# Kernel optimization log

Measured on AMD Instinct MI355X. Metric: run time of the kernel, lower is better.

Reference implementation:

```python
import jax, jax.numpy as jnp
import numpy as np

B, DETER, STOCH, ACT_DIM, HIDDEN, BLOCKS, DEMB = 4096, 4096, 1024, 32, 512, 8, 16
EPS = 1e-4
OUT_B = DETER // BLOCKS            # 512 per-block output
IN_B0 = 4 * HIDDEN + OUT_B          # 2560 per-block input of first hidden block-GEMM


def rmsnorm(x, g):
    return x * jax.lax.rsqrt(jnp.mean(x * x, axis=-1, keepdims=True) + EPS) * g


def setup_inputs() -> dict:
    key = jax.random.key(0)
    ks = jax.random.split(key, 16)
    n = lambda k, s: (jax.random.normal(k, s, jnp.float32) * 0.02)
    return {
        'stoch': jax.random.normal(ks[0], (B, STOCH), jnp.float32),
        'deter': jax.random.normal(ks[1], (B, DETER), jnp.float32),
        'action': jax.random.normal(ks[2], (B, ACT_DIM), jnp.float32),
        'd_emb': jax.random.normal(ks[3], (B, DEMB), jnp.float32),
        # four input branches: Linear -> RMSNorm -> SiLU
        'W0': n(ks[4], (DETER, HIDDEN)), 'b0': jnp.zeros(HIDDEN), 'g0': jnp.ones(HIDDEN),
        'W1': n(ks[5], (STOCH, HIDDEN)), 'b1': jnp.zeros(HIDDEN), 'g1': jnp.ones(HIDDEN),
        'W2': n(ks[6], (ACT_DIM, HIDDEN)), 'b2': jnp.zeros(HIDDEN), 'g2': jnp.ones(HIDDEN),
        'W3': n(ks[7], (DEMB, HIDDEN)), 'b3': jnp.zeros(HIDDEN), 'g3': jnp.ones(HIDDEN),
        # block-diagonal hidden layers (dynlayers=2)
        'Wh0': n(ks[8], (BLOCKS, IN_B0, OUT_B)), 'bh0': jnp.zeros(DETER), 'gh0': jnp.ones(DETER),
        'Wh1': n(ks[9], (BLOCKS, OUT_B, OUT_B)), 'bh1': jnp.zeros(DETER), 'gh1': jnp.ones(DETER),
        # block-diagonal GRU gate projection: deter -> 3*deter
        'Wg': n(ks[10], (BLOCKS, OUT_B, 3 * OUT_B)), 'bg': jnp.zeros(3 * DETER),
    }


def reference(stoch, deter, action, d_emb,
              W0, b0, g0, W1, b1, g1, W2, b2, g2, W3, b3, g3,
              Wh0, bh0, gh0, Wh1, bh1, gh1, Wg, bg):
    act = jax.nn.silu
    Bsz = action.shape[0]
    stoch = stoch.reshape(Bsz, -1)
    # action / clip(|action|, min=1).detach()
    action = action / jax.lax.stop_gradient(jnp.maximum(jnp.abs(action), 1.0))

    x0 = act(rmsnorm(deter @ W0 + b0, g0))
    x1 = act(rmsnorm(stoch @ W1 + b1, g1))
    x2 = act(rmsnorm(action @ W2 + b2, g2))
    x3 = act(rmsnorm(d_emb @ W3 + b3, g3))
    x = jnp.concatenate([x0, x1, x2, x3], axis=-1)          # [B, 4H]

    xg = jnp.broadcast_to(x[:, None, :], (Bsz, BLOCKS, 4 * HIDDEN))
    dg = deter.reshape(Bsz, BLOCKS, OUT_B)                   # flat2group(deter)
    h = jnp.concatenate([dg, xg], axis=-1)                   # [B, blocks, in_b0]

    # hidden layer 0: BlockLinear -> RMSNorm(full width) -> act
    h = jnp.einsum('bgi,gio->bgo', h, Wh0).reshape(Bsz, DETER) + bh0
    h = act(rmsnorm(h, gh0))
    # hidden layer 1
    h = jnp.einsum('bgi,gio->bgo', h.reshape(Bsz, BLOCKS, OUT_B), Wh1).reshape(Bsz, DETER) + bh1
    h = act(rmsnorm(h, gh1))

    # GRU gates via block-diagonal GEMM: [B, blocks, 3*out_b]
    gates = jnp.einsum('bgi,gio->bgo', h.reshape(Bsz, BLOCKS, OUT_B), Wg).reshape(Bsz, 3 * DETER) + bg
    gg = gates.reshape(Bsz, BLOCKS, 3 * OUT_B)
    reset = gg[..., :OUT_B].reshape(Bsz, DETER)
    cand = gg[..., OUT_B:2 * OUT_B].reshape(Bsz, DETER)
    update = gg[..., 2 * OUT_B:].reshape(Bsz, DETER)

    reset = jax.nn.sigmoid(reset)
    cand = jnp.tanh(reset * cand)
    update = jax.nn.sigmoid(update - 1.0)
    return update * cand + (1.0 - update) * deter
```

## Files before the change

### kernel.cpp

```cpp
#include <hip/hip_runtime.h>
#include <hip/hip_bf16.h>
#include <cstdint>

typedef __bf16 bf16x8 __attribute__((ext_vector_type(8)));
typedef float f32x4 __attribute__((ext_vector_type(4)));
typedef unsigned short u16x8 __attribute__((ext_vector_type(8)));
typedef unsigned short u16x4 __attribute__((ext_vector_type(4)));

__device__ __forceinline__ unsigned short f2bf(float f) {
  unsigned int u = __float_as_uint(f);
  u += 0x7FFFu + ((u >> 16) & 1u);
  return (unsigned short)(u >> 16);
}
__device__ __forceinline__ float bf2f(unsigned short h) {
  return __uint_as_float(((unsigned int)h) << 16);
}
__device__ __forceinline__ float frcp_(float x) { return __builtin_amdgcn_rcpf(x); }
__device__ __forceinline__ float sigmoid_fast(float x) { return frcp_(1.f + __expf(-x)); }
__device__ __forceinline__ float tanh_fast(float x) { return 1.f - 2.f * frcp_(__expf(2.f * x) + 1.f); }
__device__ __forceinline__ float siluf_(float x) { return x * sigmoid_fast(x); }

#define GLOAD_LDS16(gsrc, ldst) \
  __builtin_amdgcn_global_load_lds((const __attribute__((address_space(1))) void*)(gsrc), \
                                   (__attribute__((address_space(3))) void*)(ldst), 16, 0, 0)

#define S_BARRIER() asm volatile("s_barrier" ::: "memory")
#define WAIT_LGKM0() do { asm volatile("s_waitcnt lgkmcnt(0)" ::: "memory"); \
                          __builtin_amdgcn_sched_barrier(0); } while (0)

__device__ __forceinline__ void xcd_tile(int& x, int& y, int& z) {
  const int gx = gridDim.x, gy = gridDim.y;
  const int nwg = gx * gy * gridDim.z;
  const int lin = (blockIdx.z * gy + blockIdx.y) * gx + blockIdx.x;
  const int cpx = nwg >> 3;
  const int t = (lin & 7) * cpx + (lin >> 3);
  x = t % gx;
  const int r = t / gx;
  y = r % gy;
  z = r / gy;
}

template<int F32>
__device__ __forceinline__ void gemm8_core(
    const unsigned short* __restrict__ A1, int lda1, int K1,
    const unsigned short* __restrict__ A2, int lda2, int K2,
    const unsigned short* __restrict__ Bt, int ldb,
    void* __restrict__ C, int ldc,
    int tm, int tn, unsigned short* lds)
{
  const int tid = threadIdx.x;
  const int lane = tid & 63;
  const int wave = tid >> 6;
  const int wm = (wave >> 2) * 128;
  const int wn = (wave & 3) * 64;
  const int frow = lane & 15;
  const int chunk16 = (lane >> 4) * 16;
  const int nt = (K1 + K2) >> 5;

  auto stageA = [&](unsigned short* dstA, int ktBase) {
    const unsigned short* Ab; int alda, kloc;
    if (ktBase >= K1) { Ab = A2; alda = lda2; kloc = ktBase - K1; }
    else              { Ab = A1; alda = lda1; kloc = ktBase; }
#pragma unroll
    for (int j = 0; j < 2; ++j) {
      int o = j * 8192 + tid * 16;
      int so = o ^ (((o >> 7) & 3) << 4);
      int row = so >> 6, cb = so & 63;
      GLOAD_LDS16(Ab + (long long)(tm + row) * alda + kloc + (cb >> 1),
                  (char*)dstA + j * 8192 + wave * 1024);
    }
  };
  auto stageB = [&](unsigned short* dstB, int ktBase) {
#pragma unroll
    for (int j = 0; j < 2; ++j) {
      int o = j * 8192 + tid * 16;
      int so = o ^ (((o >> 7) & 3) << 4);
      int row = so >> 6, cb = so & 63;
      GLOAD_LDS16(Bt + (long long)(tn + row) * ldb + ktBase + (cb >> 1),
                  (char*)dstB + j * 8192 + wave * 1024);
    }
  };
  auto ldswz = [&](const unsigned short* rg, int row) -> bf16x8 {
    int o = row * 64 + chunk16;
    o ^= ((o >> 7) & 3) << 4;
    return *(const bf16x8*)((const char*)rg + o);
  };

  f32x4 acc[8][4] = {};

  unsigned short* pc = lds;
  unsigned short* pn = lds + 16384;
  unsigned short* pf = lds + 32768;

  stageA(pc, 0); stageB(pc + 8192, 0);
  stageA(pn, 32); stageB(pn + 8192, 32);
  asm volatile("s_waitcnt vmcnt(4)" ::: "memory");
  S_BARRIER();

  for (int T = 0; T < nt; ++T) {
    const unsigned short* A_ = pc;
    const unsigned short* B_ = pc + 8192;
    bf16x8 av[4], bv[4];
#pragma unroll
    for (int j = 0; j < 4; ++j) bv[j] = ldswz(B_, wn + j * 16 + frow);
#pragma unroll
    for (int i = 0; i < 4; ++i) av[i] = ldswz(A_, wm + i * 16 + frow);
    if (T + 2 < nt) stageA(pf, (T + 2) * 32);
    S_BARRIER();
    WAIT_LGKM0();
    __builtin_amdgcn_s_setprio(1);
#pragma unroll
    for (int i = 0; i < 4; ++i)
#pragma unroll
      for (int j = 0; j < 4; ++j)
        acc[i][j] = __builtin_amdgcn_mfma_f32_16x16x32_bf16(av[i], bv[j], acc[i][j], 0, 0, 0);
    __builtin_amdgcn_s_setprio(0);
    __builtin_amdgcn_sched_barrier(0);
    S_BARRIER();
#pragma unroll
    for (int i = 0; i < 4; ++i) av[i] = ldswz(A_, wm + 64 + i * 16 + frow);
    if (T + 2 < nt) {
      stageB(pf + 8192, (T + 2) * 32);
      asm volatile("s_waitcnt vmcnt(4)" ::: "memory");
    } else if (T + 1 < nt) {
      asm volatile("s_waitcnt vmcnt(0)" ::: "memory");
    }
    S_BARRIER();
    WAIT_LGKM0();
    __builtin_amdgcn_s_setprio(1);
#pragma unroll
    for (int i = 0; i < 4; ++i)
#pragma unroll
      for (int j = 0; j < 4; ++j)
        acc[4 + i][j] = __builtin_amdgcn_mfma_f32_16x16x32_bf16(av[i], bv[j], acc[4 + i][j], 0, 0, 0);
    __builtin_amdgcn_s_setprio(0);
    __builtin_amdgcn_sched_barrier(0);
    S_BARRIER();
    unsigned short* t = pc; pc = pn; pn = pf; pf = t;
  }

  const int cr = (lane >> 4) * 4;
  const int cc = lane & 15;
#pragma unroll
  for (int mf = 0; mf < 8; ++mf) {
    const int r0 = tm + wm + mf * 16 + cr;
#pragma unroll
    for (int j = 0; j < 4; ++j) {
      const int col = tn + wn + j * 16 + cc;
#pragma unroll
      for (int i = 0; i < 4; ++i) {
        if (F32) ((float*)C)[(long long)(r0 + i) * ldc + col] = acc[mf][j][i];
        else ((unsigned short*)C)[(long long)(r0 + i) * ldc + col] = f2bf(acc[mf][j][i]);
      }
    }
  }
}

__global__ __launch_bounds__(512, 2) void gemm8(
    const unsigned short* __restrict__ A1, int lda1, long long a1_bs, int K1,
    const unsigned short* __restrict__ A2, int lda2, int K2,
    const unsigned short* __restrict__ Bt, int ldb, long long bt_bs,
    unsigned short* __restrict__ C, int ldc, long long c_bs)
{
  __shared__ unsigned short lds[3 * 16384];
  int tx, ty, g;
  xcd_tile(tx, ty, g);
  gemm8_core<0>(A1 + (long long)g * a1_bs, lda1, K1, A2, lda2, K2,
                Bt + (long long)g * bt_bs, ldb,
                C + (long long)g * c_bs, ldc,
                ty * 256, tx * 256, lds);
}

struct BCfg { const unsigned short* A; int lda; const unsigned short* Bt; int ldb; float* C; };
struct BPack { BCfg c[5]; };
__global__ __launch_bounds__(512, 2) void gemm8_branch(BPack p) {
  __shared__ unsigned short lds[3 * 16384];
  int tx, ty, z;
  xcd_tile(tx, ty, z);
  BCfg c = p.c[z];
  gemm8_core<1>(c.A, c.lda, 1024, nullptr, 0, 0, c.Bt, c.ldb, c.C, 512,
                ty * 256, tx * 256, lds);
}

__global__ __launch_bounds__(512, 2) void gemm_gru(
    const unsigned short* __restrict__ hB,
    const unsigned short* __restrict__ Wgt,
    const float* __restrict__ bg,
    const unsigned short* __restrict__ deterB,
    float* __restrict__ out)
{
  __shared__ unsigned short lds[3 * 14336];
  int txi, tyi, g;
  xcd_tile(txi, tyi, g);
  const int tm = tyi * 256;
  const int tn = txi * 192;
  const unsigned short* A  = hB + g * 512;
  const unsigned short* Bt = Wgt + (long long)g * 1536 * 512;
  const int tid = threadIdx.x, lane = tid & 63, wave = tid >> 6;
  const int wm = (wave >> 2) * 128;
  const int wv = wave & 3;
  const int frow = lane & 15, chunk16 = (lane >> 4) * 16;
  const bool wlow = (wave < 4);
  const int nt = 16;

  auto stageA = [&](unsigned short* buf, int kt) {
#pragma unroll
    for (int j = 0; j < 2; ++j) {
      int o = j * 8192 + tid * 16;
      int so = o ^ (((o >> 7) & 3) << 4);
      int row = so >> 6, cb = so & 63;
      GLOAD_LDS16(A + (long long)(tm + row) * 4096 + kt + (cb >> 1),
                  (char*)buf + j * 8192 + wave * 1024);
    }
  };
  auto stageB = [&](unsigned short* buf, int kt) {
    char* bb = (char*)(buf + 8192);
    {
      int o = tid * 16;
      int so = o ^ (((o >> 7) & 3) << 4);
      int row = so >> 6, cb = so & 63;
      GLOAD_LDS16(Bt + (long long)(tn + row) * 512 + kt + (cb >> 1),
                  bb + wave * 1024);
    }
    if (tid < 256) {
      int o = 8192 + tid * 16;
      int so = o ^ (((o >> 7) & 3) << 4);
      int row = so >> 6, cb = so & 63;
      GLOAD_LDS16(Bt + (long long)(tn + row) * 512 + kt + (cb >> 1),
                  bb + 8192 + wave * 1024);
    }
  };
  auto ldA = [&](const unsigned short* buf, int row) -> bf16x8 {
    int o = row * 64 + chunk16; o ^= ((o >> 7) & 3) << 4;
    return *(const bf16x8*)((const char*)buf + o);
  };
  auto ldB = [&](const unsigned short* buf, int nf) -> bf16x8 {
    int row = wv * 48 + nf * 16 + frow;
    int o = row * 64 + chunk16; o ^= ((o >> 7) & 3) << 4;
    return *(const bf16x8*)((const char*)(buf + 8192) + o);
  };
  auto wait_pref = [&]() {
    if (wlow) asm volatile("s_waitcnt vmcnt(4)" ::: "memory");
    else      asm volatile("s_waitcnt vmcnt(3)" ::: "memory");
  };

  f32x4 acc[8][3] = {};

  unsigned short* pc = lds;
  unsigned short* pn = lds + 14336;
  unsigned short* pf = lds + 28672;

  stageA(pc, 0); stageB(pc, 0);
  stageA(pn, 32); stageB(pn, 32);
  wait_pref();
  S_BARRIER();

  for (int T = 0; T < nt; ++T) {
    bf16x8 av[4], bv[3];
#pragma unroll
    for (int j = 0; j < 3; ++j) bv[j] = ldB(pc, j);
#pragma unroll
    for (int i = 0; i < 4; ++i) av[i] = ldA(pc, wm + i * 16 + frow);
    if (T + 2 < nt) stageA(pf, (T + 2) * 32);
    S_BARRIER();
    WAIT_LGKM0();
    __builtin_amdgcn_s_setprio(1);
#pragma unroll
    for (int i = 0; i < 4; ++i)
#pragma unroll
      for (int j = 0; j < 3; ++j)
        acc[i][j] = __builtin_amdgcn_mfma_f32_16x16x32_bf16(av[i], bv[j], acc[i][j], 0, 0, 0);
    __builtin_amdgcn_s_setprio(0);
    __builtin_amdgcn_sched_barrier(0);
    S_BARRIER();
#pragma unroll
    for (int i = 0; i < 4; ++i) av[i] = ldA(pc, wm + 64 + i * 16 + frow);
    if (T + 2 < nt) {
      stageB(pf, (T + 2) * 32);
      wait_pref();
    } else if (T + 1 < nt) {
      asm volatile("s_waitcnt vmcnt(0)" ::: "memory");
    }
    S_BARRIER();
    WAIT_LGKM0();
    __builtin_amdgcn_s_setprio(1);
#pragma unroll
    for (int i = 0; i < 4; ++i)
#pragma unroll
      for (int j = 0; j < 3; ++j)
        acc[4 + i][j] = __builtin_amdgcn_mfma_f32_16x16x32_bf16(av[i], bv[j], acc[4 + i][j], 0, 0, 0);
    __builtin_amdgcn_s_setprio(0);
    __builtin_amdgcn_sched_barrier(0);
    S_BARRIER();
    unsigned short* t = pc; pc = pn; pn = pf; pf = t;
  }

  const int cr = (lane >> 4) * 4, cc = lane & 15;
  const int o_col = (txi * 4 + wv) * 16 + cc;
  const int gcol = g * 512 + o_col;
  const float bgr = bg[g * 1536 + o_col];
  const float bgc = bg[g * 1536 + 512 + o_col];
  const float bgu = bg[g * 1536 + 1024 + o_col];
#pragma unroll
  for (int mf = 0; mf < 8; ++mf) {
    const int r0 = tm + wm + mf * 16 + cr;
#pragma unroll
    for (int i = 0; i < 4; ++i) {
      const long long off = (long long)(r0 + i) * 4096 + gcol;
      float dt = bf2f(deterB[off]);
      float reset = sigmoid_fast(acc[mf][0][i] + bgr);
      float cand  = tanh_fast(reset * (acc[mf][1][i] + bgc));
      float upd   = sigmoid_fast(acc[mf][2][i] + bgu - 1.f);
      out[off] = upd * cand + (1.f - upd) * dt;
    }
  }
}

__global__ void cvt2_bf16_k(const float* __restrict__ sa, unsigned short* __restrict__ da, int n4a,
                            const float* __restrict__ sb, unsigned short* __restrict__ db, int n4b) {
  int i = blockIdx.x * 256 + threadIdx.x;
  const float* s; unsigned short* d;
  if (i < n4a) { s = sa; d = da; }
  else { i -= n4a; if (i >= n4b) return; s = sb; d = db; }
  float4 v = ((const float4*)s)[i];
  u16x4 o;
  o.x = f2bf(v.x); o.y = f2bf(v.y); o.z = f2bf(v.z); o.w = f2bf(v.w);
  ((u16x4*)d)[i] = o;
}

__global__ void transpose_cvt(const float* __restrict__ src, unsigned short* __restrict__ dst,
                              int R, int C) {
  __shared__ float t[32][33];
  const long long bOff = (long long)blockIdx.z * R * C;
  src += bOff; dst += bOff;
  const int c0 = blockIdx.x * 32, r0 = blockIdx.y * 32;
  const int tx = threadIdx.x, ty = threadIdx.y;
#pragma unroll
  for (int i = 0; i < 4; ++i) {
    int r = r0 + ty + i * 8, c = c0 + tx;
    if (r < R && c < C) t[ty + i * 8][tx] = src[(long long)r * C + c];
  }
  __syncthreads();
#pragma unroll
  for (int i = 0; i < 4; ++i) {
    int c = c0 + ty + i * 8, r = r0 + tx;
    if (r < R && c < C) dst[(long long)c * R + r] = f2bf(t[tx][ty + i * 8]);
  }
}

__global__ void transpose_wg(const float* __restrict__ src, unsigned short* __restrict__ dst) {
  __shared__ float t[32][33];
  const int gz = blockIdx.z;
  src += (long long)gz * 512 * 1536;
  dst += (long long)gz * 1536 * 512;
  const int c0 = blockIdx.x * 32, r0 = blockIdx.y * 32;
  const int tx = threadIdx.x, ty = threadIdx.y;
#pragma unroll
  for (int i = 0; i < 4; ++i)
    t[ty + i * 8][tx] = src[(long long)(r0 + ty + i * 8) * 1536 + c0 + tx];
  __syncthreads();
#pragma unroll
  for (int i = 0; i < 4; ++i) {
    int c = c0 + ty + i * 8;
    int gate = c >> 9, o = c & 511;
    int nn = (o >> 4) * 48 + gate * 16 + (o & 15);
    dst[(long long)nn * 512 + r0 + tx] = f2bf(t[tx][ty + i * 8]);
  }
}

__global__ __launch_bounds__(256) void branch_epi_k(
    const float* __restrict__ yP0, const float* __restrict__ yP1,
    const float* __restrict__ b0, const float* __restrict__ g0,
    const float* __restrict__ b1, const float* __restrict__ g1,
    const float* __restrict__ action, const float* __restrict__ demb,
    const float* __restrict__ W2, const float* __restrict__ b2, const float* __restrict__ g2,
    const float* __restrict__ W3, const float* __restrict__ b3, const float* __restrict__ g3,
    unsigned short* __restrict__ x)
{
  const int row = blockIdx.x, br = blockIdx.y;
  const int tid = threadIdx.x, lane = tid & 63, wave = tid >> 6;
  __shared__ float red[4];
  __shared__ float a[32];
  float v0, v1;
  const float* gg;
  if (br == 0) {
    const float* p = yP0 + (long long)row * 512;
    v0 = b0[tid]; v1 = b0[tid + 256];
#pragma unroll
    for (int c = 0; c < 4; ++c) {
      v0 += p[c * 2097152 + tid];
      v1 += p[c * 2097152 + tid + 256];
    }
    gg = g0;
  } else if (br == 1) {
    const float* p = yP1 + (long long)row * 512;
    v0 = b1[tid] + p[tid];
    v1 = b1[tid + 256] + p[tid + 256];
    gg = g1;
  } else {
    const int K = (br == 3) ? 16 : 32;
    const float* W  = (br == 3) ? W3 : W2;
    const float* bb = (br == 3) ? b3 : b2;
    gg = (br == 3) ? g3 : g2;
    if (tid < K) {
      float t = (br == 3) ? demb[(long long)row * 16 + tid]
                          : action[(long long)row * 32 + tid];
      if (br == 2) t = t / fmaxf(fabsf(t), 1.f);
      a[tid] = t;
    }
    __syncthreads();
    v0 = bb[tid]; v1 = bb[tid + 256];
    for (int k = 0; k < K; ++k) {
      float av = a[k];
      v0 += av * W[k * 512 + tid];
      v1 += av * W[k * 512 + tid + 256];
    }
  }
  float ss = v0 * v0 + v1 * v1;
  for (int o = 32; o > 0; o >>= 1) ss += __shfl_xor(ss, o);
  if (lane == 0) red[wave] = ss;
  __syncthreads();
  float ms = (red[0] + red[1] + red[2] + red[3]) * (1.f / 512.f);
  float sc = rsqrtf(ms + 1e-4f);
  unsigned short* xr = x + (long long)row * 2048 + br * 512;
  xr[tid]       = f2bf(siluf_(v0 * sc * gg[tid]));
  xr[tid + 256] = f2bf(siluf_(v1 * sc * gg[tid + 256]));
}

__global__ __launch_bounds__(256) void epi_full_k(
    const unsigned short* __restrict__ y, const float* __restrict__ bias,
    const float* __restrict__ gw, unsigned short* __restrict__ h)
{
  const int row = blockIdx.x;
  __shared__ float red[4];
  const int tid = threadIdx.x, lane = tid & 63, wave = tid >> 6;
  const u16x8* yv = (const u16x8*)(y + (long long)row * 4096);
  u16x8 ta = yv[tid], tb = yv[256 + tid];
  float ba[8], bb8[8];
  *(float4*)&ba[0]  = *(const float4*)&bias[tid * 8];
  *(float4*)&ba[4]  = *(const float4*)&bias[tid * 8 + 4];
  *(float4*)&bb8[0] = *(const float4*)&bias[(256 + tid) * 8];
  *(float4*)&bb8[4] = *(const float4*)&bias[(256 + tid) * 8 + 4];
  float fa[8], fb[8];
  float ss = 0.f;
#pragma unroll
  for (int e = 0; e < 8; ++e) {
    fa[e] = bf2f(ta[e]) + ba[e];  ss += fa[e] * fa[e];
    fb[e] = bf2f(tb[e]) + bb8[e]; ss += fb[e] * fb[e];
  }
  for (int o = 32; o > 0; o >>= 1) ss += __shfl_xor(ss, o);
  if (lane == 0) red[wave] = ss;
  __syncthreads();
  float ms = (red[0] + red[1] + red[2] + red[3]) * (1.f / 4096.f);
  float sc = rsqrtf(ms + 1e-4f);
  float ga[8], gb8[8];
  *(float4*)&ga[0]  = *(const float4*)&gw[tid * 8];
  *(float4*)&ga[4]  = *(const float4*)&gw[tid * 8 + 4];
  *(float4*)&gb8[0] = *(const float4*)&gw[(256 + tid) * 8];
  *(float4*)&gb8[4] = *(const float4*)&gw[(256 + tid) * 8 + 4];
  u16x8 oa, ob;
#pragma unroll
  for (int e = 0; e < 8; ++e) {
    oa[e] = f2bf(siluf_(fa[e] * sc * ga[e]));
    ob[e] = f2bf(siluf_(fb[e] * sc * gb8[e]));
  }
  u16x8* hv = (u16x8*)(h + (long long)row * 4096);
  hv[tid] = oa;
  hv[256 + tid] = ob;
}

extern "C" void kernel_launch(void* const* d_in, const int* in_sizes, int n_in,
                              void* d_out, int out_size, void* d_ws, size_t ws_size,
                              hipStream_t stream) {
  const float* stoch  = (const float*)d_in[0];
  const float* deter  = (const float*)d_in[1];
  const float* action = (const float*)d_in[2];
  const float* demb   = (const float*)d_in[3];
  const float* W0 = (const float*)d_in[4];
  const float* b0 = (const float*)d_in[5];
  const float* g0 = (const float*)d_in[6];
  const float* W1 = (const float*)d_in[7];
  const float* b1 = (const float*)d_in[8];
  const float* g1 = (const float*)d_in[9];
  const float* W2 = (const float*)d_in[10];
  const float* b2 = (const float*)d_in[11];
  const float* g2 = (const float*)d_in[12];
  const float* W3 = (const float*)d_in[13];
  const float* b3 = (const float*)d_in[14];
  const float* g3 = (const float*)d_in[15];
  const float* Wh0 = (const float*)d_in[16];
  const float* bh0 = (const float*)d_in[17];
  const float* gh0 = (const float*)d_in[18];
  const float* Wh1 = (const float*)d_in[19];
  const float* bh1 = (const float*)d_in[20];
  const float* gh1 = (const float*)d_in[21];
  const float* Wg  = (const float*)d_in[22];
  const float* bg  = (const float*)d_in[23];
  float* out = (float*)d_out;

  char* ws = (char*)d_ws;
  unsigned short* deterB = (unsigned short*)(ws + 0);
  unsigned short* stochB = (unsigned short*)(ws + 33554432);
  unsigned short* W0t    = (unsigned short*)(ws + 41943040);
  unsigned short* W1t    = (unsigned short*)(ws + 46137344);
  unsigned short* xB     = (unsigned short*)(ws + 47185920);
  float*          yP0    = (float*)(ws + 63963136);
  unsigned short* yB     = (unsigned short*)(ws + 63963136);
  float*          yP1    = (float*)(ws + 97517568);
  unsigned short* Wh0t   = (unsigned short*)(ws + 105906176);
  unsigned short* Wgt    = (unsigned short*)(ws + 105906176);
  unsigned short* Wh1t   = (unsigned short*)(ws + 126877696);
  unsigned short* hB     = (unsigned short*)(ws + 134217728);
  (void)in_sizes; (void)n_in; (void)out_size; (void)ws_size;

  dim3 b256(256);
  dim3 b512(512);
  dim3 tb(32, 8);
  cvt2_bf16_k<<<dim3(20480), b256, 0, stream>>>(deter, deterB, 4194304,
                                                stoch, stochB, 1048576);
  transpose_cvt<<<dim3(16, 128, 1), tb, 0, stream>>>(W0,  W0t,  4096, 512);
  transpose_cvt<<<dim3(16, 32, 1),  tb, 0, stream>>>(W1,  W1t,  1024, 512);
  {
    BPack p;
    for (int z = 0; z < 4; ++z)
      p.c[z] = { deterB + z * 1024, 4096, W0t + z * 1024, 4096, yP0 + (long long)z * 2097152 };
    p.c[4] = { stochB, 1024, W1t, 1024, yP1 };
    gemm8_branch<<<dim3(2, 16, 5), b512, 0, stream>>>(p);
  }
  branch_epi_k<<<dim3(4096, 4), b256, 0, stream>>>(yP0, yP1, b0, g0, b1, g1,
                                                   action, demb, W2, b2, g2, W3, b3, g3, xB);
  transpose_cvt<<<dim3(16, 80, 8),  tb, 0, stream>>>(Wh0, Wh0t, 2560, 512);
  transpose_cvt<<<dim3(16, 16, 8),  tb, 0, stream>>>(Wh1, Wh1t, 512,  512);
  gemm8<<<dim3(2, 16, 8), b512, 0, stream>>>(deterB, 4096, 512, 512, xB, 2048, 2048,
                                             Wh0t, 2560, 512LL * 2560, yB, 4096, 512);
  transpose_wg<<<dim3(48, 16, 8), tb, 0, stream>>>(Wg, Wgt);
  epi_full_k<<<dim3(4096), b256, 0, stream>>>(yB, bh0, gh0, hB);
  gemm8<<<dim3(2, 16, 8), b512, 0, stream>>>(hB, 4096, 512, 512, nullptr, 0, 0,
                                             Wh1t, 512, 512LL * 512, yB, 4096, 512);
  epi_full_k<<<dim3(4096), b256, 0, stream>>>(yB, bh1, gh1, hB);
  gemm_gru<<<dim3(8, 16, 8), b512, 0, stream>>>(hB, Wgt, bg, deterB, out);
}
```

Before: 336.0 us.

## Simplify GEMM pipeline barriers, rebalance split-K branch GEMM, vectorize weight transposes

The GEMM main loop now issues both A and B stages for tile T+2 up front and keeps a single barrier per K-step, where before it had several barriers between the two MFMA halves. The deter branch GEMM is split-K across six uneven K chunks instead of four, giving more workgroups, and the epilogue sums the two extra partial buffers. The weight transpose kernels now use 128-column tiles with float4 loads and packed 4-element bf16 stores. Fewer barriers risk less latency hiding or LDS hazards, and the extra partials add memory traffic in the epilogue.

```diff
diff --git a/kernel.cpp b/kernel.cpp
--- a/kernel.cpp
+++ b/kernel.cpp
@@ -98,15 +98,12 @@
   S_BARRIER();
 
   for (int T = 0; T < nt; ++T) {
-    const unsigned short* A_ = pc;
-    const unsigned short* B_ = pc + 8192;
     bf16x8 av[4], bv[4];
 #pragma unroll
-    for (int j = 0; j < 4; ++j) bv[j] = ldswz(B_, wn + j * 16 + frow);
-#pragma unroll
-    for (int i = 0; i < 4; ++i) av[i] = ldswz(A_, wm + i * 16 + frow);
-    if (T + 2 < nt) stageA(pf, (T + 2) * 32);
-    S_BARRIER();
+    for (int j = 0; j < 4; ++j) bv[j] = ldswz(pc + 8192, wn + j * 16 + frow);
+#pragma unroll
+    for (int i = 0; i < 4; ++i) av[i] = ldswz(pc, wm + i * 16 + frow);
+    if (T + 2 < nt) { stageA(pf, (T + 2) * 32); stageB(pf + 8192, (T + 2) * 32); }
     WAIT_LGKM0();
     __builtin_amdgcn_s_setprio(1);
 #pragma unroll
@@ -116,16 +113,8 @@
         acc[i][j] = __builtin_amdgcn_mfma_f32_16x16x32_bf16(av[i], bv[j], acc[i][j], 0, 0, 0);
     __builtin_amdgcn_s_setprio(0);
     __builtin_amdgcn_sched_barrier(0);
-    S_BARRIER();
-#pragma unroll
-    for (int i = 0; i < 4; ++i) av[i] = ldswz(A_, wm + 64 + i * 16 + frow);
-    if (T + 2 < nt) {
-      stageB(pf + 8192, (T + 2) * 32);
-      asm volatile("s_waitcnt vmcnt(4)" ::: "memory");
-    } else if (T + 1 < nt) {
-      asm volatile("s_waitcnt vmcnt(0)" ::: "memory");
-    }
-    S_BARRIER();
+#pragma unroll
+    for (int i = 0; i < 4; ++i) av[i] = ldswz(pc, wm + 64 + i * 16 + frow);
     WAIT_LGKM0();
     __builtin_amdgcn_s_setprio(1);
 #pragma unroll
@@ -135,6 +124,8 @@
         acc[4 + i][j] = __builtin_amdgcn_mfma_f32_16x16x32_bf16(av[i], bv[j], acc[4 + i][j], 0, 0, 0);
     __builtin_amdgcn_s_setprio(0);
     __builtin_amdgcn_sched_barrier(0);
+    if (T + 2 < nt) asm volatile("s_waitcnt vmcnt(4)" ::: "memory");
+    else            asm volatile("s_waitcnt vmcnt(0)" ::: "memory");
     S_BARRIER();
     unsigned short* t = pc; pc = pn; pn = pf; pf = t;
   }
@@ -171,14 +162,15 @@
                 ty * 256, tx * 256, lds);
 }
 
-struct BCfg { const unsigned short* A; int lda; const unsigned short* Bt; int ldb; float* C; };
-struct BPack { BCfg c[5]; };
+struct BCfg { const unsigned short* A; int lda; int K;
+              const unsigned short* Bt; int ldb; float* C; };
+struct BPack { BCfg c[7]; };
 __global__ __launch_bounds__(512, 2) void gemm8_branch(BPack p) {
   __shared__ unsigned short lds[3 * 16384];
   int tx, ty, z;
   xcd_tile(tx, ty, z);
   BCfg c = p.c[z];
-  gemm8_core<1>(c.A, c.lda, 1024, nullptr, 0, 0, c.Bt, c.ldb, c.C, 512,
+  gemm8_core<1>(c.A, c.lda, c.K, nullptr, 0, 0, c.Bt, c.ldb, c.C, 512,
                 ty * 256, tx * 256, lds);
 }
 
@@ -328,48 +320,65 @@
   ((u16x4*)d)[i] = o;
 }
 
-__global__ void transpose_cvt(const float* __restrict__ src, unsigned short* __restrict__ dst,
-                              int R, int C) {
-  __shared__ float t[32][33];
+__global__ __launch_bounds__(256) void transpose_cvt(
+    const float* __restrict__ src, unsigned short* __restrict__ dst, int R, int C) {
+  __shared__ float t[32][132];
   const long long bOff = (long long)blockIdx.z * R * C;
   src += bOff; dst += bOff;
-  const int c0 = blockIdx.x * 32, r0 = blockIdx.y * 32;
-  const int tx = threadIdx.x, ty = threadIdx.y;
-#pragma unroll
-  for (int i = 0; i < 4; ++i) {
-    int r = r0 + ty + i * 8, c = c0 + tx;
-    if (r < R && c < C) t[ty + i * 8][tx] = src[(long long)r * C + c];
+  const int c0 = blockIdx.x * 128, r0 = blockIdx.y * 32;
+  const int tid = threadIdx.x;
+  const int tx = tid & 31, ty = tid >> 5;
+#pragma unroll
+  for (int j = 0; j < 4; ++j) {
+    int row = ty + j * 8;
+    float4 v = *(const float4*)&src[(long long)(r0 + row) * C + c0 + tx * 4];
+    *(float4*)&t[row][tx * 4] = v;
   }
   __syncthreads();
 #pragma unroll
-  for (int i = 0; i < 4; ++i) {
-    int c = c0 + ty + i * 8, r = r0 + tx;
-    if (r < R && c < C) dst[(long long)c * R + r] = f2bf(t[tx][ty + i * 8]);
-  }
-}
-
-__global__ void transpose_wg(const float* __restrict__ src, unsigned short* __restrict__ dst) {
-  __shared__ float t[32][33];
+  for (int j = 0; j < 4; ++j) {
+    int idx = j * 256 + tid;
+    int c = idx >> 3, rg = idx & 7;
+    u16x4 o;
+    o.x = f2bf(t[rg * 4 + 0][c]); o.y = f2bf(t[rg * 4 + 1][c]);
+    o.z = f2bf(t[rg * 4 + 2][c]); o.w = f2bf(t[rg * 4 + 3][c]);
+    *(u16x4*)&dst[(long long)(c0 + c) * R + r0 + rg * 4] = o;
+  }
+}
+
+__global__ __launch_bounds__(256) void transpose_wg(
+    const float* __restrict__ src, unsigned short* __restrict__ dst) {
+  __shared__ float t[32][132];
   const int gz = blockIdx.z;
   src += (long long)gz * 512 * 1536;
   dst += (long long)gz * 1536 * 512;
-  const int c0 = blockIdx.x * 32, r0 = blockIdx.y * 32;
-  const int tx = threadIdx.x, ty = threadIdx.y;
-#pragma unroll
-  for (int i = 0; i < 4; ++i)
-    t[ty + i * 8][tx] = src[(long long)(r0 + ty + i * 8) * 1536 + c0 + tx];
+  const int c0 = blockIdx.x * 128, r0 = blockIdx.y * 32;
+  const int tid = threadIdx.x;
+  const int tx = tid & 31, ty = tid >> 5;
+#pragma unroll
+  for (int j = 0; j < 4; ++j) {
+    int row = ty + j * 8;
+    float4 v = *(const float4*)&src[(long long)(r0 + row) * 1536 + c0 + tx * 4];
+    *(float4*)&t[row][tx * 4] = v;
+  }
   __syncthreads();
 #pragma unroll
-  for (int i = 0; i < 4; ++i) {
-    int c = c0 + ty + i * 8;
-    int gate = c >> 9, o = c & 511;
+  for (int j = 0; j < 4; ++j) {
+    int idx = j * 256 + tid;
+    int c = idx >> 3, rg = idx & 7;
+    int cc = c0 + c;
+    int gate = cc >> 9, o = cc & 511;
     int nn = (o >> 4) * 48 + gate * 16 + (o & 15);
-    dst[(long long)nn * 512 + r0 + tx] = f2bf(t[tx][ty + i * 8]);
+    u16x4 oo;
+    oo.x = f2bf(t[rg * 4 + 0][c]); oo.y = f2bf(t[rg * 4 + 1][c]);
+    oo.z = f2bf(t[rg * 4 + 2][c]); oo.w = f2bf(t[rg * 4 + 3][c]);
+    *(u16x4*)&dst[(long long)nn * 512 + r0 + rg * 4] = oo;
   }
 }
 
 __global__ __launch_bounds__(256) void branch_epi_k(
-    const float* __restrict__ yP0, const float* __restrict__ yP1,
+    const float* __restrict__ yP0, const float* __restrict__ yPx,
+    const float* __restrict__ yP1,
     const float* __restrict__ b0, const float* __restrict__ g0,
     const float* __restrict__ b1, const float* __restrict__ g1,
     const float* __restrict__ action, const float* __restrict__ demb,
@@ -385,11 +394,17 @@
   const float* gg;
   if (br == 0) {
     const float* p = yP0 + (long long)row * 512;
+    const float* q = yPx + (long long)row * 512;
     v0 = b0[tid]; v1 = b0[tid + 256];
 #pragma unroll
     for (int c = 0; c < 4; ++c) {
       v0 += p[c * 2097152 + tid];
       v1 += p[c * 2097152 + tid + 256];
+    }
+#pragma unroll
+    for (int c = 0; c < 2; ++c) {
+      v0 += q[c * 2097152 + tid];
+      v1 += q[c * 2097152 + tid + 256];
     }
     gg = g0;
   } else if (br == 1) {
@@ -511,29 +526,34 @@
   unsigned short* Wgt    = (unsigned short*)(ws + 105906176);
   unsigned short* Wh1t   = (unsigned short*)(ws + 126877696);
   unsigned short* hB     = (unsigned short*)(ws + 134217728);
+  float*          yPx    = (float*)(ws + 134217728);
   (void)in_sizes; (void)n_in; (void)out_size; (void)ws_size;
 
   dim3 b256(256);
   dim3 b512(512);
-  dim3 tb(32, 8);
   cvt2_bf16_k<<<dim3(20480), b256, 0, stream>>>(deter, deterB, 4194304,
                                                 stoch, stochB, 1048576);
-  transpose_cvt<<<dim3(16, 128, 1), tb, 0, stream>>>(W0,  W0t,  4096, 512);
-  transpose_cvt<<<dim3(16, 32, 1),  tb, 0, stream>>>(W1,  W1t,  1024, 512);
+  transpose_cvt<<<dim3(4, 128, 1), b256, 0, stream>>>(W0,  W0t,  4096, 512);
+  transpose_cvt<<<dim3(4, 32, 1),  b256, 0, stream>>>(W1,  W1t,  1024, 512);
   {
+    const int k0s[6]   = {0, 704, 1408, 2112, 2784, 3456};
+    const int klen[6]  = {704, 704, 704, 672, 672, 640};
     BPack p;
-    for (int z = 0; z < 4; ++z)
-      p.c[z] = { deterB + z * 1024, 4096, W0t + z * 1024, 4096, yP0 + (long long)z * 2097152 };
-    p.c[4] = { stochB, 1024, W1t, 1024, yP1 };
-    gemm8_branch<<<dim3(2, 16, 5), b512, 0, stream>>>(p);
-  }
-  branch_epi_k<<<dim3(4096, 4), b256, 0, stream>>>(yP0, yP1, b0, g0, b1, g1,
+    for (int z = 0; z < 6; ++z) {
+      float* part = (z < 4) ? (yP0 + (long long)z * 2097152)
+                            : (yPx + (long long)(z - 4) * 2097152);
+      p.c[z] = { deterB + k0s[z], 4096, klen[z], W0t + k0s[z], 4096, part };
+    }
+    p.c[6] = { stochB, 1024, 1024, W1t, 1024, yP1 };
+    gemm8_branch<<<dim3(2, 16, 7), b512, 0, stream>>>(p);
+  }
+  branch_epi_k<<<dim3(4096, 4), b256, 0, stream>>>(yP0, yPx, yP1, b0, g0, b1, g1,
                                                    action, demb, W2, b2, g2, W3, b3, g3, xB);
-  transpose_cvt<<<dim3(16, 80, 8),  tb, 0, stream>>>(Wh0, Wh0t, 2560, 512);
-  transpose_cvt<<<dim3(16, 16, 8),  tb, 0, stream>>>(Wh1, Wh1t, 512,  512);
+  transpose_cvt<<<dim3(4, 80, 8),  b256, 0, stream>>>(Wh0, Wh0t, 2560, 512);
+  transpose_cvt<<<dim3(4, 16, 8),  b256, 0, stream>>>(Wh1, Wh1t, 512,  512);
   gemm8<<<dim3(2, 16, 8), b512, 0, stream>>>(deterB, 4096, 512, 512, xB, 2048, 2048,
                                              Wh0t, 2560, 512LL * 2560, yB, 4096, 512);
-  transpose_wg<<<dim3(48, 16, 8), tb, 0, stream>>>(Wg, Wgt);
+  transpose_wg<<<dim3(12, 16, 8), b256, 0, stream>>>(Wg, Wgt);
   epi_full_k<<<dim3(4096), b256, 0, stream>>>(yB, bh0, gh0, hB);
   gemm8<<<dim3(2, 16, 8), b512, 0, stream>>>(hB, 4096, 512, 512, nullptr, 0, 0,
                                              Wh1t, 512, 512LL * 512, yB, 4096, 512);
```

After: 329.3 us. 2.0% less time.
